# Kernel optimization log

Hardware: AMD Instinct MI355X
Metric: run time of the kernel (lower is better)

Reference implementation:

```python
import jax, jax.numpy as jnp
import numpy as np

B, S, D, H, DK = 2, 2048, 1024, 16, 64  # d_model = n_heads * d_k

def setup_inputs() -> dict:
    key = jax.random.key(0)
    ks = jax.random.split(key, 11)
    s = 1.0 / np.sqrt(D)
    return {
        "Q": jax.random.normal(ks[0], (B, S, D), jnp.float32),
        "K": jax.random.normal(ks[1], (B, S, D), jnp.float32),
        "V": jax.random.normal(ks[2], (B, S, D), jnp.float32),
        "wq": jax.random.normal(ks[3], (D, D), jnp.float32) * s,
        "bq": jnp.zeros((D,), jnp.float32),
        "wk": jax.random.normal(ks[4], (D, D), jnp.float32) * s,
        "bk": jnp.zeros((D,), jnp.float32),
        "wv": jax.random.normal(ks[5], (D, D), jnp.float32) * s,
        "bv": jnp.zeros((D,), jnp.float32),
        "wo": jax.random.normal(ks[6], (D, D), jnp.float32) * s,
        "bo": jnp.zeros((D,), jnp.float32),
    }

def reference(Q, K, V, wq, bq, wk, bk, wv, bv, wo, bo):
    # linear projections (torch Linear: x @ W^T + b)
    q = Q @ wq.T + bq
    k = K @ wk.T + bk
    v = V @ wv.T + bv
    # split heads -> [B, H, S, DK]
    def split(t):
        return t.reshape(B, S, H, DK).transpose(0, 2, 1, 3)
    q, k, v = split(q), split(k), split(v)
    scale = 1.0 / np.sqrt(DK)
    scores = jnp.einsum('bhqd,bhkd->bhqk', q, k) * scale  # [B,H,S,S]
    probs = jax.nn.softmax(scores, axis=-1)
    # dropout is identity in eval mode
    ctx = jnp.einsum('bhqk,bhkd->bhqd', probs, v)  # [B,H,S,DK]
    ctx = ctx.transpose(0, 2, 1, 3).reshape(B, S, D)
    return ctx @ wo.T + bo
```

## Files before the change

### kernel.cpp

```cpp
#include <hip/hip_runtime.h>

#define S_LEN 2048
#define DMODEL 1024
#define DHEAD 64

typedef _Float16 half8 __attribute__((ext_vector_type(8)));
typedef _Float16 half4 __attribute__((ext_vector_type(4)));
typedef float f32x4 __attribute__((ext_vector_type(4)));
typedef int i32x4 __attribute__((ext_vector_type(4)));

#define LOG2E 1.4426950408889634f

__device__ __forceinline__ void async_copy16(const void* g, void* l) {
  __builtin_amdgcn_global_load_lds((__attribute__((address_space(1))) const void*)g,
                                   (__attribute__((address_space(3))) void*)l,
                                   16, 0, 0);
}

#define WAIT_VMCNT(N) asm volatile("s_waitcnt vmcnt(" #N ")" ::: "memory")
#define WAIT_LGKM0() asm volatile("s_waitcnt lgkmcnt(0)" ::: "memory")
#define RAW_BARRIER() asm volatile("s_barrier" ::: "memory")

__global__ __launch_bounds__(256) void convert_w(const float* __restrict__ wq,
                                                 const float* __restrict__ wk,
                                                 const float* __restrict__ wv,
                                                 _Float16* __restrict__ dst) {
  const float* src = (blockIdx.y == 0) ? wq : (blockIdx.y == 1) ? wk : wv;
  _Float16* d = dst + (size_t)blockIdx.y * (DMODEL * DMODEL);
  int i = (blockIdx.x * 256 + threadIdx.x) * 4;
  float4 v = *(const float4*)(src + i);
  half4 h;
  h[0] = (_Float16)v.x; h[1] = (_Float16)v.y;
  h[2] = (_Float16)v.z; h[3] = (_Float16)v.w;
  *(half4*)(d + i) = h;
}

__global__ __launch_bounds__(256) void convert_wo(const float* __restrict__ wo,
                                                  _Float16* __restrict__ dst) {
  int i = (blockIdx.x * 256 + threadIdx.x) * 4;
  float4 v = *(const float4*)(wo + i);
  half4 h;
  h[0] = (_Float16)v.x; h[1] = (_Float16)v.y;
  h[2] = (_Float16)v.z; h[3] = (_Float16)v.w;
  *(half4*)(dst + i) = h;
}

__global__ __launch_bounds__(256, 3) void qkv_gemm(
    const float* __restrict__ Qf, const float* __restrict__ Kf, const float* __restrict__ Vf,
    const _Float16* __restrict__ wh,
    const float* __restrict__ bq, const float* __restrict__ bk, const float* __restrict__ bv,
    _Float16* __restrict__ qo, _Float16* __restrict__ ko, _Float16* __restrict__ vt) {
  __shared__ __align__(16) _Float16 Asb[2][128 * 32];
  __shared__ __align__(16) _Float16 Bsb[3][128 * 32];
  const int tid = threadIdx.x;
  const int wave = tid >> 6, lane = tid & 63;
  const int m15 = lane & 15, quad = lane >> 4;
  const int m0 = blockIdx.x * 128;
  const int gn0 = blockIdx.y * 128;
  const int sel = gn0 >> 10;
  const int n0 = gn0 & 1023;
  const float* Ag = (sel == 0) ? Qf : (sel == 1) ? Kf : Vf;
  const _Float16* Wg = wh + (size_t)sel * (DMODEL * DMODEL);
  const float* bias = (sel == 0) ? bq : (sel == 1) ? bk : bv;

  const int wm = (wave & 1) * 64, wn = (wave >> 1) * 64;

  const int sr = tid >> 1, sc16 = (tid & 1) * 16;
  const int g0 = (tid & 1) * 2, asw = (sr >> 1) & 3;
  const int b_r = lane >> 2, b_g = (lane & 3) ^ ((lane >> 3) & 3);
  const int ra = ((quad ^ ((m15 >> 1) & 3)) << 4);

  f32x4 acc[4][4];
#pragma unroll
  for (int i = 0; i < 4; i++)
#pragma unroll
    for (int j = 0; j < 4; j++) {
      f32x4 z = {0.f, 0.f, 0.f, 0.f};
      acc[i][j] = z;
    }

  const float* ap = Ag + (size_t)(m0 + sr) * DMODEL + sc16;
  float4 f0, f1, f2, f3;

  auto loadA = [&](int kk) {
    const float* p = ap + kk;
    f0 = ((const float4*)p)[0];
    f1 = ((const float4*)p)[1];
    f2 = ((const float4*)p)[2];
    f3 = ((const float4*)p)[3];
  };
  auto writeA = [&](int nb) {
    half8 h0, h1;
    h0[0] = (_Float16)f0.x; h0[1] = (_Float16)f0.y; h0[2] = (_Float16)f0.z; h0[3] = (_Float16)f0.w;
    h0[4] = (_Float16)f1.x; h0[5] = (_Float16)f1.y; h0[6] = (_Float16)f1.z; h0[7] = (_Float16)f1.w;
    h1[0] = (_Float16)f2.x; h1[1] = (_Float16)f2.y; h1[2] = (_Float16)f2.z; h1[3] = (_Float16)f2.w;
    h1[4] = (_Float16)f3.x; h1[5] = (_Float16)f3.y; h1[6] = (_Float16)f3.z; h1[7] = (_Float16)f3.w;
    char* rb = (char*)&Asb[nb][0] + sr * 64;
    *(half8*)(rb + ((g0 ^ asw) << 4)) = h0;
    *(half8*)(rb + (((g0 + 1) ^ asw) << 4)) = h1;
  };
  auto issueB = [&](int kk, int nb) {
#pragma unroll
    for (int p = 0; p < 2; p++) {
      int row = (p * 4 + wave) * 16 + b_r;
      async_copy16(Wg + (size_t)(n0 + row) * DMODEL + kk + b_g * 8,
                   (char*)&Bsb[nb][0] + p * 4096 + wave * 1024);
    }
  };

  loadA(0);
  issueB(0, 0);
  issueB(32, 1);
  WAIT_VMCNT(4);
  writeA(0);
  WAIT_VMCNT(2);
  WAIT_LGKM0();
  RAW_BARRIER();

  int bcur = 0, bnxt = 2;
  for (int kt = 0; kt < 32; kt++) {
    const int bufA = kt & 1;
    if (kt < 31) loadA((kt + 1) * 32);
    if (kt < 30) issueB((kt + 2) * 32, bnxt);

    const char* ab = (const char*)&Asb[bufA][0];
    const char* bb = (const char*)&Bsb[bcur][0];
    half8 af[4], bf[4];
#pragma unroll
    for (int i = 0; i < 4; i++)
      af[i] = *(const half8*)(ab + (wm + i * 16 + m15) * 64 + ra);
#pragma unroll
    for (int j = 0; j < 4; j++)
      bf[j] = *(const half8*)(bb + (wn + j * 16 + m15) * 64 + ra);
#pragma unroll
    for (int i = 0; i < 4; i++)
#pragma unroll
      for (int j = 0; j < 4; j++)
        acc[i][j] = __builtin_amdgcn_mfma_f32_16x16x32_f16(af[i], bf[j], acc[i][j], 0, 0, 0);

    if (kt == 31) break;
    if (kt < 30) { WAIT_VMCNT(2); } else { WAIT_VMCNT(0); }
    writeA(bufA ^ 1);
    WAIT_LGKM0();
    RAW_BARRIER();
    bcur = (bcur == 2) ? 0 : bcur + 1;
    bnxt = (bnxt == 2) ? 0 : bnxt + 1;
  }
  if (sel != 2) {
    _Float16* outp = (sel == 0) ? qo : ko;
    const float scale = (sel == 0) ? (0.125f * LOG2E) : 1.0f;
#pragma unroll
    for (int i = 0; i < 4; i++) {
#pragma unroll
      for (int j = 0; j < 4; j++) {
        int gn = n0 + wn + j * 16 + m15;
        float bb = bias[gn];
#pragma unroll
        for (int r = 0; r < 4; r++) {
          int gm = m0 + wm + i * 16 + quad * 4 + r;
          outp[(size_t)gm * DMODEL + gn] = (_Float16)((acc[i][j][r] + bb) * scale);
        }
      }
    }
  } else {
#pragma unroll
    for (int i = 0; i < 4; i++) {
      int gm0 = m0 + wm + i * 16 + quad * 4;
      int b = gm0 >> 11, s = gm0 & 2047;
#pragma unroll
      for (int j = 0; j < 4; j++) {
        int gn = n0 + wn + j * 16 + m15;
        int h = gn >> 6, dk = gn & 63;
        float bb = bias[gn];
        half4 hv;
        hv[0] = (_Float16)(acc[i][j][0] + bb);
        hv[1] = (_Float16)(acc[i][j][1] + bb);
        hv[2] = (_Float16)(acc[i][j][2] + bb);
        hv[3] = (_Float16)(acc[i][j][3] + bb);
        *(half4*)(vt + ((size_t)(b * 16 + h) * 64 + dk) * 2048 + s) = hv;
      }
    }
  }
}

__global__ __launch_bounds__(256) void attn_kernel(const _Float16* __restrict__ qh,
                                                   const _Float16* __restrict__ kh,
                                                   const _Float16* __restrict__ vt,
                                                   _Float16* __restrict__ ctx) {
  __shared__ __align__(16) char smem[49152];
  const int tid = threadIdx.x;
  const int wave = tid >> 6, lane = tid & 63;
  const int m15 = lane & 15, qd = lane >> 4;
  const int wq = wave >> 1, ws = wave & 1;
  const int q0 = blockIdx.x * 64;
  const int h = blockIdx.y, b = blockIdx.z;
  const size_t base = (size_t)b * S_LEN * DMODEL + (size_t)h * DHEAD;
  const size_t vbase = (size_t)(b * 16 + h) * 64 * 2048;

  half8 qf[2][2];
#pragma unroll
  for (int qt = 0; qt < 2; qt++) {
    const _Float16* qp = qh + base + (size_t)(q0 + wq * 32 + qt * 16 + m15) * DMODEL + qd * 8;
    qf[qt][0] = *(const half8*)qp;
    qf[qt][1] = *(const half8*)(qp + 32);
  }

  const int l8 = lane >> 3, s8 = lane & 7;
  const int swz = (s8 ^ l8) * 8;
  const _Float16* ksrc = kh + base + (size_t)(wave * 8 + l8) * DMODEL + swz;
  const _Float16* vsrc = vt + vbase + (size_t)(wave * 8 + l8) * S_LEN + swz;

  const int kgr = ((qd ^ (m15 & 7)) << 4);
  const int vgr = (((ws * 4 + qd) ^ (m15 & 7)) << 4);
  const int krow = ws * 32 + m15;

  auto stage = [&](int tile, int bufi) {
    const int kv = tile * 64;
    char* kd = smem + bufi * 8192 + wave * 1024;
    char* vd = smem + 24576 + bufi * 8192 + wave * 1024;
#pragma unroll
    for (int p = 0; p < 2; p++) {
      async_copy16(ksrc + (size_t)(kv + p * 32) * DMODEL, kd + p * 4096);
      async_copy16(vsrc + (size_t)(p * 32) * S_LEN + kv, vd + p * 4096);
    }
  };

  f32x4 acc[4][2];
#pragma unroll
  for (int i = 0; i < 4; i++)
#pragma unroll
    for (int j = 0; j < 2; j++) { f32x4 z = {0.f, 0.f, 0.f, 0.f}; acc[i][j] = z; }
  float ls[2] = {0.f, 0.f};

  stage(0, 0);
  stage(1, 1);
  WAIT_VMCNT(4);
  RAW_BARRIER();

  int bcur = 0, bnxt = 2;
  for (int it = 0; it < 32; it++) {
    if (it < 30) stage(it + 2, bnxt);
    const char* kb = smem + bcur * 8192;
    const char* vb = smem + 24576 + bcur * 8192;

    half8 kf[2][2];
#pragma unroll
    for (int t = 0; t < 2; t++) {
      kf[t][0] = *(const half8*)(kb + (krow + 16 * t) * 128 + kgr);
      kf[t][1] = *(const half8*)(kb + (krow + 16 * t) * 128 + (kgr ^ 64));
    }

    f32x4 sc[2][2];
#pragma unroll
    for (int t = 0; t < 2; t++)
#pragma unroll
      for (int qt = 0; qt < 2; qt++) {
        f32x4 z = {0.f, 0.f, 0.f, 0.f};
        sc[t][qt] = __builtin_amdgcn_mfma_f32_16x16x32_f16(kf[t][0], qf[qt][0], z, 0, 0, 0);
        sc[t][qt] = __builtin_amdgcn_mfma_f32_16x16x32_f16(kf[t][1], qf[qt][1], sc[t][qt], 0, 0, 0);
      }

    int pk[2][2][2];
#pragma unroll
    for (int t = 0; t < 2; t++)
#pragma unroll
      for (int qt = 0; qt < 2; qt++) {
        float e0 = __builtin_amdgcn_exp2f(sc[t][qt][0]);
        float e1 = __builtin_amdgcn_exp2f(sc[t][qt][1]);
        float e2 = __builtin_amdgcn_exp2f(sc[t][qt][2]);
        float e3 = __builtin_amdgcn_exp2f(sc[t][qt][3]);
        ls[qt] += (e0 + e1) + (e2 + e3);
        pk[t][qt][0] = __builtin_bit_cast(int, __builtin_amdgcn_cvt_pkrtz(e0, e1));
        pk[t][qt][1] = __builtin_bit_cast(int, __builtin_amdgcn_cvt_pkrtz(e2, e3));
      }

    half8 pA[2];
#pragma unroll
    for (int qt = 0; qt < 2; qt++) {
      i32x4 fh;
#pragma unroll
      for (int p = 0; p < 2; p++) {
        auto s1 = __builtin_amdgcn_permlane32_swap(pk[0][qt][p], pk[1][qt][p], false, false);
        auto s2 = __builtin_amdgcn_permlane16_swap(s1[0], s1[1], false, false);
        fh[p] = (int)s2[0];
        fh[2 + p] = (int)s2[1];
      }
      pA[qt] = __builtin_bit_cast(half8, fh);
    }

#pragma unroll
    for (int td = 0; td < 4; td++) {
      half8 vf = *(const half8*)(vb + (td * 16 + m15) * 128 + vgr);
#pragma unroll
      for (int qt = 0; qt < 2; qt++)
        acc[td][qt] = __builtin_amdgcn_mfma_f32_16x16x32_f16(vf, pA[qt], acc[td][qt], 0, 0, 0);
    }
    if (it < 30) { WAIT_VMCNT(4); } else { WAIT_VMCNT(0); }
    RAW_BARRIER();
    bcur = (bcur == 2) ? 0 : bcur + 1;
    bnxt = (bnxt == 2) ? 0 : bnxt + 1;
  }

  float* Ored = (float*)smem;
  float* Lred = (float*)(smem + 17408);

#pragma unroll
  for (int qt = 0; qt < 2; qt++) {
    ls[qt] += __shfl_xor(ls[qt], 16);
    ls[qt] += __shfl_xor(ls[qt], 32);
  }

  if (ws == 1) {
#pragma unroll
    for (int qt = 0; qt < 2; qt++) {
      int q = wq * 32 + qt * 16 + m15;
      if (qd == 0) Lred[q] = ls[qt];
#pragma unroll
      for (int td = 0; td < 4; td++)
        *(f32x4*)&Ored[q * 68 + td * 16 + qd * 4] = acc[td][qt];
    }
  }
  __syncthreads();

  if (ws == 0) {
#pragma unroll
    for (int qt = 0; qt < 2; qt++) {
      int q = wq * 32 + qt * 16 + m15;
      const float inv = 1.0f / (ls[qt] + Lred[q]);
#pragma unroll
      for (int td = 0; td < 4; td++) {
        f32x4 o = acc[td][qt] + *(const f32x4*)&Ored[q * 68 + td * 16 + qd * 4];
        half4 hv;
#pragma unroll
        for (int r = 0; r < 4; r++) hv[r] = (_Float16)(o[r] * inv);
        *(half4*)(ctx + base + (size_t)(q0 + q) * DMODEL + td * 16 + qd * 4) = hv;
      }
    }
  }
}

__global__ __launch_bounds__(256, 4) void out_gemm(const _Float16* __restrict__ ch,
                                                   const _Float16* __restrict__ who,
                                                   const float* __restrict__ bo,
                                                   float* __restrict__ out) {
  __shared__ __align__(16) _Float16 As[2][64 * 32];
  __shared__ __align__(16) _Float16 Bs[2][128 * 32];
  const int tid = threadIdx.x;
  const int wave = tid >> 6, lane = tid & 63;
  const int m15 = lane & 15, quad = lane >> 4;
  const int m0 = blockIdx.x * 64, n0 = blockIdx.y * 128;
  const int wm = (wave & 1) * 32, wn = (wave >> 1) * 64;
  const int b_r = lane >> 2, b_g = (lane & 3) ^ ((lane >> 3) & 3);
  const int rgr = ((quad ^ ((m15 >> 1) & 3)) << 4);

  f32x4 acc[2][4];
#pragma unroll
  for (int i = 0; i < 2; i++)
#pragma unroll
    for (int j = 0; j < 4; j++) {
      f32x4 z = {0.f, 0.f, 0.f, 0.f};
      acc[i][j] = z;
    }

  auto issueTile = [&](int kk, int nb) {
    {
      int row = wave * 16 + b_r;
      async_copy16(ch + (size_t)(m0 + row) * DMODEL + kk + b_g * 8,
                   (char*)&As[nb][0] + wave * 1024);
    }
#pragma unroll
    for (int p = 0; p < 2; p++) {
      int row = (p * 4 + wave) * 16 + b_r;
      async_copy16(who + (size_t)(n0 + row) * DMODEL + kk + b_g * 8,
                   (char*)&Bs[nb][0] + p * 4096 + wave * 1024);
    }
  };

  issueTile(0, 0);
  issueTile(32, 1);
  WAIT_VMCNT(3);
  RAW_BARRIER();

  for (int kt = 0; kt < 32; kt++) {
    const int buf = kt & 1;
    half8 af[2], bf[4];
#pragma unroll
    for (int i = 0; i < 2; i++)
      af[i] = *(const half8*)((char*)&As[buf][0] + (wm + i * 16 + m15) * 64 + rgr);
#pragma unroll
    for (int j = 0; j < 4; j++)
      bf[j] = *(const half8*)((char*)&Bs[buf][0] + (wn + j * 16 + m15) * 64 + rgr);
#pragma unroll
    for (int i = 0; i < 2; i++)
#pragma unroll
      for (int j = 0; j < 4; j++)
        acc[i][j] = __builtin_amdgcn_mfma_f32_16x16x32_f16(af[i], bf[j], acc[i][j], 0, 0, 0);
    if (kt == 31) break;
    RAW_BARRIER();
    if (kt < 30) {
      issueTile((kt + 2) * 32, buf);
      WAIT_VMCNT(3);
    } else {
      WAIT_VMCNT(0);
    }
    RAW_BARRIER();
  }
#pragma unroll
  for (int i = 0; i < 2; i++) {
#pragma unroll
    for (int j = 0; j < 4; j++) {
      int gn = n0 + wn + j * 16 + m15;
      float bb = bo[gn];
#pragma unroll
      for (int r = 0; r < 4; r++) {
        int gm = m0 + wm + i * 16 + quad * 4 + r;
        out[(size_t)gm * DMODEL + gn] = acc[i][j][r] + bb;
      }
    }
  }
}

extern "C" void kernel_launch(void* const* d_in, const int* in_sizes, int n_in,
                              void* d_out, int out_size, void* d_ws, size_t ws_size,
                              hipStream_t stream) {
  (void)in_sizes; (void)n_in; (void)out_size; (void)ws_size;
  const float* Q  = (const float*)d_in[0];
  const float* K  = (const float*)d_in[1];
  const float* V  = (const float*)d_in[2];
  const float* wq = (const float*)d_in[3];
  const float* bq = (const float*)d_in[4];
  const float* wk = (const float*)d_in[5];
  const float* bk = (const float*)d_in[6];
  const float* wv = (const float*)d_in[7];
  const float* bv = (const float*)d_in[8];
  const float* wo = (const float*)d_in[9];
  const float* bo = (const float*)d_in[10];
  float* out = (float*)d_out;

  _Float16* qh = (_Float16*)d_out;
  _Float16* kh = qh + (size_t)4194304;
  _Float16* vt = (_Float16*)d_ws;
  _Float16* wh = vt + (size_t)4194304;
  _Float16* ch = vt + (size_t)4194304;
  _Float16* who = (_Float16*)d_ws;

  convert_w<<<dim3(1024, 3), 256, 0, stream>>>(wq, wk, wv, wh);
  qkv_gemm<<<dim3(32, 24), 256, 0, stream>>>(Q, K, V, wh, bq, bk, bv, qh, kh, vt);
  attn_kernel<<<dim3(32, 16, 2), 256, 0, stream>>>(qh, kh, vt, ch);
  convert_wo<<<dim3(1024), 256, 0, stream>>>(wo, who);
  out_gemm<<<dim3(64, 8), 256, 0, stream>>>(ch, who, bo, out);
}
```

Before: 239.2 us.

## Use 512-thread blocks in QKV GEMM with deeper A prefetch and V-first ordering

```diff
diff --git a/kernel.cpp b/kernel.cpp
--- a/kernel.cpp
+++ b/kernel.cpp
@@ -45,7 +45,7 @@
   *(half4*)(dst + i) = h;
 }
 
-__global__ __launch_bounds__(256, 3) void qkv_gemm(
+__global__ __launch_bounds__(512, 4) void qkv_gemm(
     const float* __restrict__ Qf, const float* __restrict__ Kf, const float* __restrict__ Vf,
     const _Float16* __restrict__ wh,
     const float* __restrict__ bq, const float* __restrict__ bk, const float* __restrict__ bv,
@@ -56,101 +56,99 @@
   const int wave = tid >> 6, lane = tid & 63;
   const int m15 = lane & 15, quad = lane >> 4;
   const int m0 = blockIdx.x * 128;
-  const int gn0 = blockIdx.y * 128;
-  const int sel = gn0 >> 10;
-  const int n0 = gn0 & 1023;
+  const int y = blockIdx.y;
+  const int sel = (y < 8) ? 2 : (y < 16) ? 0 : 1;
+  const int n0 = (y & 7) * 128;
   const float* Ag = (sel == 0) ? Qf : (sel == 1) ? Kf : Vf;
   const _Float16* Wg = wh + (size_t)sel * (DMODEL * DMODEL);
   const float* bias = (sel == 0) ? bq : (sel == 1) ? bk : bv;
 
-  const int wm = (wave & 1) * 64, wn = (wave >> 1) * 64;
-
-  const int sr = tid >> 1, sc16 = (tid & 1) * 16;
-  const int g0 = (tid & 1) * 2, asw = (sr >> 1) & 3;
-  const int b_r = lane >> 2, b_g = (lane & 3) ^ ((lane >> 3) & 3);
+  const int wm = (wave & 3) * 32, wn = (wave >> 2) * 64;
+
+  const int sr = tid >> 2, c4 = tid & 3;
+  const int aslot = ((c4 ^ ((sr >> 1) & 3)) << 4);
+  const int b_g = (lane & 3) ^ ((lane >> 3) & 3);
   const int ra = ((quad ^ ((m15 >> 1) & 3)) << 4);
 
-  f32x4 acc[4][4];
-#pragma unroll
-  for (int i = 0; i < 4; i++)
+  f32x4 acc[2][4];
+#pragma unroll
+  for (int i = 0; i < 2; i++)
 #pragma unroll
     for (int j = 0; j < 4; j++) {
       f32x4 z = {0.f, 0.f, 0.f, 0.f};
       acc[i][j] = z;
     }
 
-  const float* ap = Ag + (size_t)(m0 + sr) * DMODEL + sc16;
-  float4 f0, f1, f2, f3;
-
-  auto loadA = [&](int kk) {
+  const float* ap = Ag + (size_t)(m0 + sr) * DMODEL + c4 * 8;
+
+  auto loadA = [&](int kk, float4 (&s)[2]) {
     const float* p = ap + kk;
-    f0 = ((const float4*)p)[0];
-    f1 = ((const float4*)p)[1];
-    f2 = ((const float4*)p)[2];
-    f3 = ((const float4*)p)[3];
-  };
-  auto writeA = [&](int nb) {
-    half8 h0, h1;
-    h0[0] = (_Float16)f0.x; h0[1] = (_Float16)f0.y; h0[2] = (_Float16)f0.z; h0[3] = (_Float16)f0.w;
-    h0[4] = (_Float16)f1.x; h0[5] = (_Float16)f1.y; h0[6] = (_Float16)f1.z; h0[7] = (_Float16)f1.w;
-    h1[0] = (_Float16)f2.x; h1[1] = (_Float16)f2.y; h1[2] = (_Float16)f2.z; h1[3] = (_Float16)f2.w;
-    h1[4] = (_Float16)f3.x; h1[5] = (_Float16)f3.y; h1[6] = (_Float16)f3.z; h1[7] = (_Float16)f3.w;
-    char* rb = (char*)&Asb[nb][0] + sr * 64;
-    *(half8*)(rb + ((g0 ^ asw) << 4)) = h0;
-    *(half8*)(rb + (((g0 + 1) ^ asw) << 4)) = h1;
+    s[0] = ((const float4*)p)[0];
+    s[1] = ((const float4*)p)[1];
+  };
+  auto writeA = [&](const float4 (&s)[2], int nb) {
+    half8 h;
+    h[0] = (_Float16)s[0].x; h[1] = (_Float16)s[0].y;
+    h[2] = (_Float16)s[0].z; h[3] = (_Float16)s[0].w;
+    h[4] = (_Float16)s[1].x; h[5] = (_Float16)s[1].y;
+    h[6] = (_Float16)s[1].z; h[7] = (_Float16)s[1].w;
+    *(half8*)((char*)&Asb[nb][0] + sr * 64 + aslot) = h;
   };
   auto issueB = [&](int kk, int nb) {
-#pragma unroll
-    for (int p = 0; p < 2; p++) {
-      int row = (p * 4 + wave) * 16 + b_r;
-      async_copy16(Wg + (size_t)(n0 + row) * DMODEL + kk + b_g * 8,
-                   (char*)&Bsb[nb][0] + p * 4096 + wave * 1024);
-    }
-  };
-
-  loadA(0);
+    int row = wave * 16 + (lane >> 2);
+    async_copy16(Wg + (size_t)(n0 + row) * DMODEL + kk + b_g * 8,
+                 (char*)&Bsb[nb][0] + wave * 1024);
+  };
+
+  float4 aE[2], aO[2];
+
+  loadA(0, aE);
+  loadA(32, aO);
   issueB(0, 0);
   issueB(32, 1);
   WAIT_VMCNT(4);
-  writeA(0);
-  WAIT_VMCNT(2);
+  writeA(aE, 0);
+  WAIT_VMCNT(1);
   WAIT_LGKM0();
   RAW_BARRIER();
 
-  int bcur = 0, bnxt = 2;
-  for (int kt = 0; kt < 32; kt++) {
-    const int bufA = kt & 1;
-    if (kt < 31) loadA((kt + 1) * 32);
-    if (kt < 30) issueB((kt + 2) * 32, bnxt);
-
-    const char* ab = (const char*)&Asb[bufA][0];
-    const char* bb = (const char*)&Bsb[bcur][0];
-    half8 af[4], bf[4];
-#pragma unroll
-    for (int i = 0; i < 4; i++)
+  auto body = [&](int kt, float4 (&cur)[2] , float4 (&nxt)[2] ) {
+    if (kt < 30) {
+      loadA((kt + 2) * 32, nxt);
+      issueB((kt + 2) * 32, (kt + 2) % 3);
+    }
+    const char* ab = (const char*)&Asb[kt & 1][0];
+    const char* bb = (const char*)&Bsb[kt % 3][0];
+    half8 af[2], bf[4];
+#pragma unroll
+    for (int i = 0; i < 2; i++)
       af[i] = *(const half8*)(ab + (wm + i * 16 + m15) * 64 + ra);
 #pragma unroll
     for (int j = 0; j < 4; j++)
       bf[j] = *(const half8*)(bb + (wn + j * 16 + m15) * 64 + ra);
 #pragma unroll
-    for (int i = 0; i < 4; i++)
+    for (int i = 0; i < 2; i++)
 #pragma unroll
       for (int j = 0; j < 4; j++)
         acc[i][j] = __builtin_amdgcn_mfma_f32_16x16x32_f16(af[i], bf[j], acc[i][j], 0, 0, 0);
-
-    if (kt == 31) break;
-    if (kt < 30) { WAIT_VMCNT(2); } else { WAIT_VMCNT(0); }
-    writeA(bufA ^ 1);
+    if (kt == 31) return;
+    if (kt < 30) { WAIT_VMCNT(3); } else { WAIT_VMCNT(0); }
+    writeA(cur, (kt + 1) & 1);
     WAIT_LGKM0();
     RAW_BARRIER();
-    bcur = (bcur == 2) ? 0 : bcur + 1;
-    bnxt = (bnxt == 2) ? 0 : bnxt + 1;
-  }
+  };
+
+#pragma unroll 1
+  for (int k2 = 0; k2 < 16; k2++) {
+    body(2 * k2, aO, aE);
+    body(2 * k2 + 1, aE, aO);
+  }
+
   if (sel != 2) {
     _Float16* outp = (sel == 0) ? qo : ko;
     const float scale = (sel == 0) ? (0.125f * LOG2E) : 1.0f;
 #pragma unroll
-    for (int i = 0; i < 4; i++) {
+    for (int i = 0; i < 2; i++) {
 #pragma unroll
       for (int j = 0; j < 4; j++) {
         int gn = n0 + wn + j * 16 + m15;
@@ -164,7 +162,7 @@
     }
   } else {
 #pragma unroll
-    for (int i = 0; i < 4; i++) {
+    for (int i = 0; i < 2; i++) {
       int gm0 = m0 + wm + i * 16 + quad * 4;
       int b = gm0 >> 11, s = gm0 & 2047;
 #pragma unroll
@@ -445,7 +443,7 @@
   _Float16* who = (_Float16*)d_ws;
 
   convert_w<<<dim3(1024, 3), 256, 0, stream>>>(wq, wk, wv, wh);
-  qkv_gemm<<<dim3(32, 24), 256, 0, stream>>>(Q, K, V, wh, bq, bk, bv, qh, kh, vt);
+  qkv_gemm<<<dim3(32, 24), 512, 0, stream>>>(Q, K, V, wh, bq, bk, bv, qh, kh, vt);
   attn_kernel<<<dim3(32, 16, 2), 256, 0, stream>>>(qh, kh, vt, ch);
   convert_wo<<<dim3(1024), 256, 0, stream>>>(wo, who);
   out_gemm<<<dim3(64, 8), 256, 0, stream>>>(ch, who, bo, out);
```

Measured after the change: 239.1 us. Within noise of the previous version (-0.0%).

## Triple-buffer GEMM pipelines and prefetch A deeper in QKV projection

Applied to the files above, without the earlier changes.

```diff
diff --git a/kernel.cpp b/kernel.cpp
--- a/kernel.cpp
+++ b/kernel.cpp
@@ -50,15 +50,15 @@
     const _Float16* __restrict__ wh,
     const float* __restrict__ bq, const float* __restrict__ bk, const float* __restrict__ bv,
     _Float16* __restrict__ qo, _Float16* __restrict__ ko, _Float16* __restrict__ vt) {
-  __shared__ __align__(16) _Float16 Asb[2][128 * 32];
+  __shared__ __align__(16) _Float16 Asb[3][128 * 32];
   __shared__ __align__(16) _Float16 Bsb[3][128 * 32];
   const int tid = threadIdx.x;
   const int wave = tid >> 6, lane = tid & 63;
   const int m15 = lane & 15, quad = lane >> 4;
   const int m0 = blockIdx.x * 128;
-  const int gn0 = blockIdx.y * 128;
-  const int sel = gn0 >> 10;
-  const int n0 = gn0 & 1023;
+  const int y = blockIdx.y;
+  const int sel = (y < 8) ? 2 : (y < 16) ? 0 : 1;
+  const int n0 = (y & 7) * 128;
   const float* Ag = (sel == 0) ? Qf : (sel == 1) ? Kf : Vf;
   const _Float16* Wg = wh + (size_t)sel * (DMODEL * DMODEL);
   const float* bias = (sel == 0) ? bq : (sel == 1) ? bk : bv;
@@ -80,21 +80,20 @@
     }
 
   const float* ap = Ag + (size_t)(m0 + sr) * DMODEL + sc16;
-  float4 f0, f1, f2, f3;
-
-  auto loadA = [&](int kk) {
+
+  auto loadA = [&](int kk, float4 (&s)[4]) {
     const float* p = ap + kk;
-    f0 = ((const float4*)p)[0];
-    f1 = ((const float4*)p)[1];
-    f2 = ((const float4*)p)[2];
-    f3 = ((const float4*)p)[3];
-  };
-  auto writeA = [&](int nb) {
+    s[0] = ((const float4*)p)[0];
+    s[1] = ((const float4*)p)[1];
+    s[2] = ((const float4*)p)[2];
+    s[3] = ((const float4*)p)[3];
+  };
+  auto writeA = [&](const float4 (&s)[4], int nb) {
     half8 h0, h1;
-    h0[0] = (_Float16)f0.x; h0[1] = (_Float16)f0.y; h0[2] = (_Float16)f0.z; h0[3] = (_Float16)f0.w;
-    h0[4] = (_Float16)f1.x; h0[5] = (_Float16)f1.y; h0[6] = (_Float16)f1.z; h0[7] = (_Float16)f1.w;
-    h1[0] = (_Float16)f2.x; h1[1] = (_Float16)f2.y; h1[2] = (_Float16)f2.z; h1[3] = (_Float16)f2.w;
-    h1[4] = (_Float16)f3.x; h1[5] = (_Float16)f3.y; h1[6] = (_Float16)f3.z; h1[7] = (_Float16)f3.w;
+    h0[0] = (_Float16)s[0].x; h0[1] = (_Float16)s[0].y; h0[2] = (_Float16)s[0].z; h0[3] = (_Float16)s[0].w;
+    h0[4] = (_Float16)s[1].x; h0[5] = (_Float16)s[1].y; h0[6] = (_Float16)s[1].z; h0[7] = (_Float16)s[1].w;
+    h1[0] = (_Float16)s[2].x; h1[1] = (_Float16)s[2].y; h1[2] = (_Float16)s[2].z; h1[3] = (_Float16)s[2].w;
+    h1[4] = (_Float16)s[3].x; h1[5] = (_Float16)s[3].y; h1[6] = (_Float16)s[3].z; h1[7] = (_Float16)s[3].w;
     char* rb = (char*)&Asb[nb][0] + sr * 64;
     *(half8*)(rb + ((g0 ^ asw) << 4)) = h0;
     *(half8*)(rb + (((g0 + 1) ^ asw) << 4)) = h1;
@@ -107,45 +106,65 @@
                    (char*)&Bsb[nb][0] + p * 4096 + wave * 1024);
     }
   };
-
-  loadA(0);
+  auto compute = [&](int m3) {
+    const char* ab = (const char*)&Asb[m3][0];
+    const char* bb = (const char*)&Bsb[m3][0];
+    half8 af[4], bf[4];
+#pragma unroll
+    for (int i = 0; i < 4; i++)
+      af[i] = *(const half8*)(ab + (wm + i * 16 + m15) * 64 + ra);
+#pragma unroll
+    for (int j = 0; j < 4; j++)
+      bf[j] = *(const half8*)(bb + (wn + j * 16 + m15) * 64 + ra);
+#pragma unroll
+    for (int i = 0; i < 4; i++)
+#pragma unroll
+      for (int j = 0; j < 4; j++)
+        acc[i][j] = __builtin_amdgcn_mfma_f32_16x16x32_f16(af[i], bf[j], acc[i][j], 0, 0, 0);
+  };
+
+  float4 s0[4], s1[4], s2[4];
+
   issueB(0, 0);
+  loadA(0, s0);
   issueB(32, 1);
-  WAIT_VMCNT(4);
-  writeA(0);
-  WAIT_VMCNT(2);
+  loadA(32, s1);
+  loadA(64, s2);
+  WAIT_VMCNT(10);
+  writeA(s0, 0);
   WAIT_LGKM0();
   RAW_BARRIER();
 
-  int bcur = 0, bnxt = 2;
-  for (int kt = 0; kt < 32; kt++) {
-    const int bufA = kt & 1;
-    if (kt < 31) loadA((kt + 1) * 32);
-    if (kt < 30) issueB((kt + 2) * 32, bnxt);
-
-    const char* ab = (const char*)&Asb[bufA][0];
-    const char* bb = (const char*)&Bsb[bcur][0];
-    half8 af[4], bf[4];
-#pragma unroll
-    for (int i = 0; i < 4; i++)
-      af[i] = *(const half8*)(ab + (wm + i * 16 + m15) * 64 + ra);
-#pragma unroll
-    for (int j = 0; j < 4; j++)
-      bf[j] = *(const half8*)(bb + (wn + j * 16 + m15) * 64 + ra);
-#pragma unroll
-    for (int i = 0; i < 4; i++)
-#pragma unroll
-      for (int j = 0; j < 4; j++)
-        acc[i][j] = __builtin_amdgcn_mfma_f32_16x16x32_f16(af[i], bf[j], acc[i][j], 0, 0, 0);
-
-    if (kt == 31) break;
-    if (kt < 30) { WAIT_VMCNT(2); } else { WAIT_VMCNT(0); }
-    writeA(bufA ^ 1);
+  auto body = [&](int kt, int m3, int bB, int bW, float4 (&ld)[4], const float4 (&wr)[4],
+                  int mode) {
+    if (mode == 0) {
+      issueB((kt + 2) * 32, bB);
+      loadA((kt + 3) * 32, ld);
+    } else if (mode == 1) {
+      issueB((kt + 2) * 32, bB);
+    }
+    compute(m3);
+    if (mode == 3) return;
+    if (mode == 0) { WAIT_VMCNT(10); }
+    else if (mode == 1) { WAIT_VMCNT(6); }
+    else { WAIT_VMCNT(0); }
+    writeA(wr, bW);
     WAIT_LGKM0();
     RAW_BARRIER();
-    bcur = (bcur == 2) ? 0 : bcur + 1;
-    bnxt = (bnxt == 2) ? 0 : bnxt + 1;
-  }
+  };
+
+#pragma unroll 1
+  for (int k3 = 0; k3 < 27; k3 += 3) {
+    body(k3 + 0, 0, 2, 1, s0, s1, 0);
+    body(k3 + 1, 1, 0, 2, s1, s2, 0);
+    body(k3 + 2, 2, 1, 0, s2, s0, 0);
+  }
+  body(27, 0, 2, 1, s0, s1, 0);
+  body(28, 1, 0, 2, s1, s2, 0);
+  body(29, 2, 1, 0, s2, s0, 1);
+  body(30, 0, 0, 1, s0, s1, 2);
+  body(31, 1, 0, 0, s0, s0, 3);
+
   if (sel != 2) {
     _Float16* outp = (sel == 0) ? qo : ko;
     const float scale = (sel == 0) ? (0.125f * LOG2E) : 1.0f;
@@ -343,8 +362,8 @@
                                                    const _Float16* __restrict__ who,
                                                    const float* __restrict__ bo,
                                                    float* __restrict__ out) {
-  __shared__ __align__(16) _Float16 As[2][64 * 32];
-  __shared__ __align__(16) _Float16 Bs[2][128 * 32];
+  __shared__ __align__(16) _Float16 As[3][64 * 32];
+  __shared__ __align__(16) _Float16 Bs[3][128 * 32];
   const int tid = threadIdx.x;
   const int wave = tid >> 6, lane = tid & 63;
   const int m15 = lane & 15, quad = lane >> 4;
@@ -375,36 +394,37 @@
                    (char*)&Bs[nb][0] + p * 4096 + wave * 1024);
     }
   };
+  auto compute = [&](int m3) {
+    half8 af[2], bf[4];
+#pragma unroll
+    for (int i = 0; i < 2; i++)
+      af[i] = *(const half8*)((char*)&As[m3][0] + (wm + i * 16 + m15) * 64 + rgr);
+#pragma unroll
+    for (int j = 0; j < 4; j++)
+      bf[j] = *(const half8*)((char*)&Bs[m3][0] + (wn + j * 16 + m15) * 64 + rgr);
+#pragma unroll
+    for (int i = 0; i < 2; i++)
+#pragma unroll
+      for (int j = 0; j < 4; j++)
+        acc[i][j] = __builtin_amdgcn_mfma_f32_16x16x32_f16(af[i], bf[j], acc[i][j], 0, 0, 0);
+  };
 
   issueTile(0, 0);
   issueTile(32, 1);
   WAIT_VMCNT(3);
   RAW_BARRIER();
 
-  for (int kt = 0; kt < 32; kt++) {
-    const int buf = kt & 1;
-    half8 af[2], bf[4];
-#pragma unroll
-    for (int i = 0; i < 2; i++)
-      af[i] = *(const half8*)((char*)&As[buf][0] + (wm + i * 16 + m15) * 64 + rgr);
-#pragma unroll
-    for (int j = 0; j < 4; j++)
-      bf[j] = *(const half8*)((char*)&Bs[buf][0] + (wn + j * 16 + m15) * 64 + rgr);
-#pragma unroll
-    for (int i = 0; i < 2; i++)
-#pragma unroll
-      for (int j = 0; j < 4; j++)
-        acc[i][j] = __builtin_amdgcn_mfma_f32_16x16x32_f16(af[i], bf[j], acc[i][j], 0, 0, 0);
-    if (kt == 31) break;
-    RAW_BARRIER();
-    if (kt < 30) {
-      issueTile((kt + 2) * 32, buf);
-      WAIT_VMCNT(3);
-    } else {
-      WAIT_VMCNT(0);
-    }
-    RAW_BARRIER();
-  }
+#pragma unroll 1
+  for (int k3 = 0; k3 < 30; k3 += 3) {
+    issueTile((k3 + 2) * 32, 2); compute(0); WAIT_VMCNT(3); RAW_BARRIER();
+    issueTile((k3 + 3) * 32, 0); compute(1); WAIT_VMCNT(3); RAW_BARRIER();
+    issueTile((k3 + 4) * 32, 1); compute(2); WAIT_VMCNT(3); RAW_BARRIER();
+  }
+  compute(0);
+  WAIT_VMCNT(0);
+  RAW_BARRIER();
+  compute(1);
+
 #pragma unroll
   for (int i = 0; i < 2; i++) {
 #pragma unroll
```

Result: faster. 232.0 us (-3.0%).
